# Performance work log

Hardware: AMD Instinct MI355X
Metric: run time of the kernel (lower is better)

## Reference

```python
import jax, jax.numpy as jnp
import numpy as np

D_MODEL = 1024
NUM_HEADS = 16
D_K = D_MODEL // NUM_HEADS
THETA = 10000.0


def _rope(x, pos):
    # x: [H, B, S, D_K]; pos: [S] int. Interleaved-pair rotation (matrix-form RoPE).
    d2 = D_K // 2
    inv_freq = THETA ** (-(2.0 * jnp.arange(d2, dtype=jnp.float32)) / D_K)  # [d2]
    ang = pos.astype(jnp.float32)[:, None] * inv_freq[None, :]              # [S, d2]
    sin, cos = jnp.sin(ang), jnp.cos(ang)
    xr = x.reshape(*x.shape[:-1], d2, 2)
    x0, x1 = xr[..., 0], xr[..., 1]
    out0 = cos * x0 - sin * x1
    out1 = sin * x0 + cos * x1
    return jnp.stack([out0, out1], axis=-1).reshape(x.shape)


def setup_inputs() -> dict:
    key = jax.random.key(0)
    ks = jax.random.split(key, 5)
    scale = 1.0 / np.sqrt(D_MODEL)
    return {
        "x": jax.random.normal(ks[0], (4, 2048, D_MODEL), dtype=jnp.float32),
        "token_positions": jnp.arange(2048, dtype=jnp.int32),
        "Wq": jax.random.normal(ks[1], (D_MODEL, D_MODEL), dtype=jnp.float32) * scale,
        "Wk": jax.random.normal(ks[2], (D_MODEL, D_MODEL), dtype=jnp.float32) * scale,
        "Wv": jax.random.normal(ks[3], (D_MODEL, D_MODEL), dtype=jnp.float32) * scale,
        "Wo": jax.random.normal(ks[4], (D_MODEL, D_MODEL), dtype=jnp.float32) * scale,
    }


def reference(x, token_positions, Wq, Wk, Wv, Wo):
    B, S, D = x.shape
    H, dk = NUM_HEADS, D_K
    # Projections (Linear stores weight [out,in], applies x @ W.T)
    def proj(W):
        return (x @ W.T).reshape(B, S, H, dk).transpose(2, 0, 1, 3)  # [H,B,S,dk]
    q, k, v = proj(Wq), proj(Wk), proj(Wv)
    q = _rope(q, token_positions)
    k = _rope(k, token_positions)
    scores = jnp.einsum("hbsd,hbtd->hbst", q, k) / jnp.sqrt(jnp.float32(dk))
    causal = jnp.tril(jnp.ones((S, S), dtype=bool))
    scores = jnp.where(causal, scores, jnp.float32(-1e9))
    attn = jax.nn.softmax(scores, axis=-1)
    out = jnp.einsum("hbst,hbtd->hbsd", attn, v)       # [H,B,S,dk]
    out = out.transpose(1, 2, 0, 3).reshape(B, S, D)   # [B,S,D]
    return out @ Wo.T
```

## Files before the change

### kernel.cpp

```cpp
#include <hip/hip_runtime.h>

typedef __bf16 bf16;
typedef bf16 bf16x8 __attribute__((ext_vector_type(8)));
typedef bf16 bf16x4 __attribute__((ext_vector_type(4)));
typedef float floatx4 __attribute__((ext_vector_type(4)));

#define D_MODEL 1024
#define SEQ     2048
#define NB      4
#define NH      16
#define DKH     64
#define ROPE_L2 0.4152410118609203f

__device__ __forceinline__ floatx4 mfma16(bf16x8 a, bf16x8 b, floatx4 c) {
  return __builtin_amdgcn_mfma_f32_16x16x32_bf16(a, b, c, 0, 0, 0);
}

__device__ __forceinline__ void gload_lds16(void* lds_uniform, const void* gsrc) {
  __builtin_amdgcn_global_load_lds(
      (__attribute__((address_space(1))) unsigned int*)(void*)(gsrc),
      (__attribute__((address_space(3))) unsigned int*)lds_uniform,
      16, 0, 0);
}

__global__ __launch_bounds__(256) void cvt_all(
    const float4* __restrict__ x,
    const float4* __restrict__ wq, const float4* __restrict__ wk,
    const float4* __restrict__ wv, const float4* __restrict__ wo,
    bf16x4* __restrict__ xb,
    bf16x4* __restrict__ b0, bf16x4* __restrict__ b1,
    bf16x4* __restrict__ b2, bf16x4* __restrict__ b3) {
  const int i = blockIdx.x * 256 + threadIdx.x;
  const float4* src;
  bf16x4* dst;
  int off;
  if (i < (1 << 21)) {
    src = x; dst = xb; off = i;
  } else {
    const int j = i - (1 << 21);
    const int widx = j >> 18;
    off = j & ((1 << 18) - 1);
    src = (widx == 0) ? wq : (widx == 1) ? wk : (widx == 2) ? wv : wo;
    dst = (widx == 0) ? b0 : (widx == 1) ? b1 : (widx == 2) ? b2 : b3;
  }
  const float4 v = src[off];
  bf16x4 o;
  o[0] = (bf16)v.x; o[1] = (bf16)v.y; o[2] = (bf16)v.z; o[3] = (bf16)v.w;
  dst[off] = o;
}

__global__ __launch_bounds__(256) void rope_table(const int* __restrict__ tokpos,
                                                  float2* __restrict__ tab) {
  const int i = blockIdx.x * 256 + threadIdx.x;
  const int s = i >> 5, i2 = i & 31;
  const float ang = (float)tokpos[s] * exp2f(-(float)i2 * ROPE_L2);
  float sn, cs;
  sincosf(ang, &sn, &cs);
  tab[i] = make_float2(sn, cs);
}

#define GEMM_ACC_DECL                              \
  floatx4 c00 = {}, c01 = {}, c02 = {}, c03 = {};  \
  floatx4 c10 = {}, c11 = {}, c12 = {}, c13 = {};  \
  floatx4 c20 = {}, c21 = {}, c22 = {}, c23 = {};  \
  floatx4 c30 = {}, c31 = {}, c32 = {}, c33 = {};

#define AS_BASE(buf) ((char*)LDSBUF + (buf) * 8192)
#define BS_BASE(buf) ((char*)LDSBUF + 16384 + (buf) * 8192)

#define GEMM_STAGE(buf, kk)                                                    \
  gload_lds16(AS_BASE(buf) + (w * 64) * 16, asrc0 + (kk));                     \
  gload_lds16(BS_BASE(buf) + (w * 64) * 16, bsrc0 + (kk));                     \
  gload_lds16(AS_BASE(buf) + (w * 64 + 256) * 16, asrc1 + (kk));               \
  gload_lds16(BS_BASE(buf) + (w * 64 + 256) * 16, bsrc1 + (kk));

#define GEMM_MAINLOOP(Aptr, Bptr)                                              \
  const int c_0 = w * 64 + lane;                                               \
  const int row0_ = c_0 >> 2, seg0_ = (c_0 & 3) ^ ((row0_ >> 1) & 3);          \
  const int c_1 = c_0 + 256;                                                   \
  const int row1_ = c_1 >> 2, seg1_ = (c_1 & 3) ^ ((row1_ >> 1) & 3);          \
  const bf16* asrc0 = (Aptr) + (size_t)(bm + row0_) * D_MODEL + seg0_ * 8;     \
  const bf16* asrc1 = (Aptr) + (size_t)(bm + row1_) * D_MODEL + seg1_ * 8;     \
  const bf16* bsrc0 = (Bptr) + (size_t)(bn + row0_) * D_MODEL + seg0_ * 8;     \
  const bf16* bsrc1 = (Bptr) + (size_t)(bn + row1_) * D_MODEL + seg1_ * 8;     \
  const int gsw = (g ^ ((r >> 1) & 3)) * 8;                                    \
  GEMM_STAGE(0, 0)                                                             \
  __syncthreads();                                                             \
  int cub = 0;                                                                 \
  for (int kt = 0; kt < 32; ++kt) {                                            \
    if (kt + 1 < 32) { GEMM_STAGE(cub ^ 1, (kt + 1) * 32) }                    \
    const bf16* Abase = (const bf16*)AS_BASE(cub) + (wr * 64 + r) * 32 + gsw;  \
    const bf16* Bbase = (const bf16*)BS_BASE(cub) + (wc * 64 + r) * 32 + gsw;  \
    bf16x8 a0 = *(const bf16x8*)(Abase + 0 * 512);                             \
    bf16x8 a1 = *(const bf16x8*)(Abase + 1 * 512);                             \
    bf16x8 a2 = *(const bf16x8*)(Abase + 2 * 512);                             \
    bf16x8 a3 = *(const bf16x8*)(Abase + 3 * 512);                             \
    bf16x8 b0 = *(const bf16x8*)(Bbase + 0 * 512);                             \
    bf16x8 b1 = *(const bf16x8*)(Bbase + 1 * 512);                             \
    bf16x8 b2 = *(const bf16x8*)(Bbase + 2 * 512);                             \
    bf16x8 b3 = *(const bf16x8*)(Bbase + 3 * 512);                             \
    __builtin_amdgcn_s_setprio(1);                                             \
    c00 = mfma16(a0, b0, c00); c01 = mfma16(a0, b1, c01);                      \
    c02 = mfma16(a0, b2, c02); c03 = mfma16(a0, b3, c03);                      \
    c10 = mfma16(a1, b0, c10); c11 = mfma16(a1, b1, c11);                      \
    c12 = mfma16(a1, b2, c12); c13 = mfma16(a1, b3, c13);                      \
    c20 = mfma16(a2, b0, c20); c21 = mfma16(a2, b1, c21);                      \
    c22 = mfma16(a2, b2, c22); c23 = mfma16(a2, b3, c23);                      \
    c30 = mfma16(a3, b0, c30); c31 = mfma16(a3, b1, c31);                      \
    c32 = mfma16(a3, b2, c32); c33 = mfma16(a3, b3, c33);                      \
    __builtin_amdgcn_s_setprio(0);                                             \
    __syncthreads();                                                           \
    cub ^= 1;                                                                  \
  }

#define QKV_WRITE(mm, nn, CV)                                                  \
  _Pragma("unroll")                                                            \
  for (int reg = 0; reg < 4; ++reg) {                                          \
    const int srow = mm * 16 + g * 4 + reg;                                    \
    const int c = wc * 64 + nn * 16 + r;                                       \
    const int s_ = (bm + wr * 64 + srow) & (SEQ - 1);                          \
    const int d_ = c & 63;                                                     \
    float v = CV[reg];                                                         \
    float pp = __shfl_xor(v, 1);                                               \
    const float2 sc2 = ropetab[s_ * 32 + (d_ >> 1)];                           \
    float res = ((d_ & 1) == 0) ? (sc2.y * v - sc2.x * pp)                     \
                                : (sc2.x * pp + sc2.y * v);                    \
    if (z == 0) res *= 0.125f;                                                 \
    *(bf16*)((char*)LDSBUF + srow * 272 + c * 2) = (bf16)res;                  \
  }

#define V_WRITE(mm, nn, CV)                                                    \
  _Pragma("unroll")                                                            \
  for (int reg = 0; reg < 4; ++reg) {                                          \
    const int crow = nn * 16 + r;                                              \
    const int s_l = wr * 64 + mm * 16 + g * 4 + reg;                           \
    *(bf16*)((char*)LDSBUF + crow * 272 + s_l * 2) = (bf16)CV[reg];            \
  }

__global__ __launch_bounds__(256, 3) void gemm_qkv(
    const bf16* __restrict__ A,
    const bf16* __restrict__ W0, const bf16* __restrict__ W1, const bf16* __restrict__ W2,
    bf16* __restrict__ Qd, bf16* __restrict__ Kd, bf16* __restrict__ Vd,
    const float2* __restrict__ ropetab) {
  __shared__ __align__(16) char LDSBUF[32768];
  const int orig = (int)(blockIdx.x + (blockIdx.y << 3) + (blockIdx.z << 9));
  const int l = (orig & 7) * 192 + (orig >> 3);
  const int z = l >> 9;
  const int bm = ((l >> 3) & 63) * 128, bn = (l & 7) * 128;
  const bf16* Bw = (z == 0) ? W0 : (z == 1) ? W1 : W2;
  const int tid = threadIdx.x, lane = tid & 63, w = tid >> 6;
  const int wr = w >> 1, wc = w & 1;
  const int r = lane & 15, g = lane >> 4;
  GEMM_ACC_DECL
  GEMM_MAINLOOP(A, Bw)

  const int hbase = bn >> 6;
  if (z < 2) {
    bf16* dst0 = (z == 0) ? Qd : Kd;
#pragma unroll
    for (int p = 0; p < 2; ++p) {
      if (wr == p) {
        QKV_WRITE(0, 0, c00) QKV_WRITE(0, 1, c01) QKV_WRITE(0, 2, c02) QKV_WRITE(0, 3, c03)
        QKV_WRITE(1, 0, c10) QKV_WRITE(1, 1, c11) QKV_WRITE(1, 2, c12) QKV_WRITE(1, 3, c13)
        QKV_WRITE(2, 0, c20) QKV_WRITE(2, 1, c21) QKV_WRITE(2, 2, c22) QKV_WRITE(2, 3, c23)
        QKV_WRITE(3, 0, c30) QKV_WRITE(3, 1, c31) QKV_WRITE(3, 2, c32) QKV_WRITE(3, 3, c33)
      }
      __syncthreads();
      const int s_r = tid >> 2, quad = tid & 3;
      const int grow = bm + p * 64 + s_r;
      const int b_ = grow >> 11, s_ = grow & (SEQ - 1);
      const int h_ = hbase + (quad >> 1);
      bf16* dstp = dst0 + ((size_t)(b_ * NH + h_) * SEQ + s_) * DKH + (quad & 1) * 32;
#pragma unroll
      for (int j = 0; j < 4; ++j)
        *(float4*)(dstp + j * 8) =
            *(const float4*)((char*)LDSBUF + s_r * 272 + quad * 64 + j * 16);
      __syncthreads();
    }
  } else {
    const int b_ = bm >> 11, sbase = bm & (SEQ - 1);
#pragma unroll
    for (int p = 0; p < 2; ++p) {
      if (wc == p) {
        V_WRITE(0, 0, c00) V_WRITE(0, 1, c01) V_WRITE(0, 2, c02) V_WRITE(0, 3, c03)
        V_WRITE(1, 0, c10) V_WRITE(1, 1, c11) V_WRITE(1, 2, c12) V_WRITE(1, 3, c13)
        V_WRITE(2, 0, c20) V_WRITE(2, 1, c21) V_WRITE(2, 2, c22) V_WRITE(2, 3, c23)
        V_WRITE(3, 0, c30) V_WRITE(3, 1, c31) V_WRITE(3, 2, c32) V_WRITE(3, 3, c33)
      }
      __syncthreads();
      const int c_r = tid >> 2, quad = tid & 3;
      const int c = p * 64 + c_r;
      const int h_ = hbase + (c >> 6), d_ = c & 63;
      bf16* dstp = Vd + ((size_t)(b_ * NH + h_) * DKH + d_) * SEQ + sbase + quad * 32;
#pragma unroll
      for (int j = 0; j < 4; ++j)
        *(float4*)(dstp + j * 8) =
            *(const float4*)((char*)LDSBUF + c_r * 272 + quad * 64 + j * 16);
      __syncthreads();
    }
  }
}

#define OUT_EPI(mm, nn, CV)                                                    \
  _Pragma("unroll")                                                            \
  for (int reg = 0; reg < 4; ++reg) {                                          \
    const int grow = bm + wr * 64 + mm * 16 + g * 4 + reg;                     \
    const int gcol = bn + wc * 64 + nn * 16 + r;                               \
    C[(size_t)grow * D_MODEL + gcol] = CV[reg];                                \
  }

__global__ __launch_bounds__(256, 3) void gemm_out(const bf16* __restrict__ A,
                                                   const bf16* __restrict__ Bw,
                                                   float* __restrict__ C) {
  __shared__ __align__(16) char LDSBUF[32768];
  const int orig = (int)(blockIdx.x + (blockIdx.y << 3));
  const int l = (orig & 7) * 64 + (orig >> 3);
  const int bm = (l >> 3) * 128, bn = (l & 7) * 128;
  const int tid = threadIdx.x, lane = tid & 63, w = tid >> 6;
  const int wr = w >> 1, wc = w & 1;
  const int r = lane & 15, g = lane >> 4;
  GEMM_ACC_DECL
  GEMM_MAINLOOP(A, Bw)
  OUT_EPI(0, 0, c00) OUT_EPI(0, 1, c01) OUT_EPI(0, 2, c02) OUT_EPI(0, 3, c03)
  OUT_EPI(1, 0, c10) OUT_EPI(1, 1, c11) OUT_EPI(1, 2, c12) OUT_EPI(1, 3, c13)
  OUT_EPI(2, 0, c20) OUT_EPI(2, 1, c21) OUT_EPI(2, 2, c22) OUT_EPI(2, 3, c23)
  OUT_EPI(3, 0, c30) OUT_EPI(3, 1, c31) OUT_EPI(3, 2, c32) OUT_EPI(3, 3, c33)
}

__global__ __launch_bounds__(256, 3) void attn128(const bf16* __restrict__ Q,
                                                  const bf16* __restrict__ Kk,
                                                  const bf16* __restrict__ Vt,
                                                  bf16* __restrict__ AO) {
  const int orig = (int)(blockIdx.x + (blockIdx.y << 4));
  const int i_ = orig >> 3;
  const int qt = 15 - (i_ >> 3);
  const int bh = (orig & 7) * 8 + (i_ & 7);
  const int b = bh >> 4, h = bh & 15;
  const int tid = threadIdx.x, lane = tid & 63, w = tid >> 6;
  const int r = lane & 15, g = lane >> 4;
  const int q0 = qt * 128 + w * 32;

  const bf16* Qb = Q + (size_t)bh * SEQ * DKH;
  const bf16* Kb = Kk + (size_t)bh * SEQ * DKH;
  const bf16* Vb = Vt + (size_t)bh * DKH * SEQ;

  __shared__ bf16 Ks[2][64 * 64];
  __shared__ bf16 Vs[2][64 * 64];
  __shared__ bf16 Ps[4][32 * 64];

  int ldsoff[2];
  const char* ksrc[2];
  const char* vsrc[2];
#pragma unroll
  for (int j = 0; j < 2; ++j) {
    const int L = (w * 64 + lane + 256 * j) * 16;
    const int S = L ^ (((L >> 7) & 7) << 4);
    ldsoff[j] = (w * 64 + 256 * j) * 16;
    ksrc[j] = (const char*)Kb + S;
    vsrc[j] = (const char*)Vb + (size_t)(S >> 7) * (SEQ * 2) + (S & 127);
  }

#define ATTN_STAGE(buf, tt)                                                   \
  _Pragma("unroll")                                                           \
  for (int j = 0; j < 2; ++j) {                                               \
    gload_lds16((char*)Ks[buf] + ldsoff[j], ksrc[j] + (size_t)(tt) * 8192);   \
    gload_lds16((char*)Vs[buf] + ldsoff[j], vsrc[j] + (size_t)(tt) * 128);    \
  }

#define SM_TILE(MASKED)                                                        \
  _Pragma("unroll")                                                            \
  for (int m = 0; m < 2; ++m) {                                                \
    const int qq_ = q0 + m * 16 + r;                                           \
    const int wl_ = m * 16 + r;                                                \
    _Pragma("unroll")                                                          \
    for (int nf = 0; nf < 4; ++nf) {                                           \
      floatx4 p;                                                               \
      _Pragma("unroll")                                                        \
      for (int reg = 0; reg < 4; ++reg) {                                      \
        float pe = exp2f(fmaf(sc[m][nf][reg], 1.442695041f, -17.31234049f));   \
        if (MASKED && (t0 + nf * 16 + g * 4 + reg > qq_)) pe = 0.f;            \
        p[reg] = pe;                                                           \
      }                                                                        \
      l2[m] += p;                                                              \
      unsigned u0, u1;                                                         \
      asm("v_cvt_pk_bf16_f32 %0, %1, %2" : "=v"(u0) : "v"(p[0]), "v"(p[1]));   \
      asm("v_cvt_pk_bf16_f32 %0, %1, %2" : "=v"(u1) : "v"(p[2]), "v"(p[3]));   \
      const int pb = (wl_ * 128 + nf * 32 + g * 8) ^ ((wl_ & 7) << 4);         \
      *(uint2*)((char*)Ps[w] + pb) = make_uint2(u0, u1);                       \
    }                                                                          \
  }

  bf16x8 qf[2][2];
#pragma unroll
  for (int m = 0; m < 2; ++m)
#pragma unroll
    for (int ks = 0; ks < 2; ++ks)
      qf[m][ks] = *(const bf16x8*)(Qb + (size_t)(q0 + m * 16 + r) * DKH + ks * 32 + g * 8);

  floatx4 o[2][4] = {};
  floatx4 l2[2] = {};

  const int nt = 2 * qt + 2;
  ATTN_STAGE(0, 0)
  __syncthreads();
  int cu = 0;
  for (int t = 0; t < nt; ++t) {
    if (t + 1 < nt) ATTN_STAGE(cu ^ 1, t + 1)
    const int t0 = t * 64;

    floatx4 sc[2][4];
    __builtin_amdgcn_s_setprio(1);
#pragma unroll
    for (int nf = 0; nf < 4; ++nf) {
      const int row = nf * 16 + r;
      const int off0 = (row * 128 + g * 16) ^ ((row & 7) << 4);
      bf16x8 kf0 = *(const bf16x8*)((const char*)Ks[cu] + off0);
      bf16x8 kf1 = *(const bf16x8*)((const char*)Ks[cu] + (off0 ^ 64));
      sc[0][nf] = mfma16(kf1, qf[0][1], mfma16(kf0, qf[0][0], floatx4{0.f, 0.f, 0.f, 0.f}));
      sc[1][nf] = mfma16(kf1, qf[1][1], mfma16(kf0, qf[1][0], floatx4{0.f, 0.f, 0.f, 0.f}));
    }
    __builtin_amdgcn_s_setprio(0);

    const bool edge = (t0 + 63 > q0);
    if (edge) {
      SM_TILE(1)
    } else {
      SM_TILE(0)
    }
    asm volatile("s_waitcnt lgkmcnt(0)" ::: "memory");

    bf16x8 pf[2][2];
#pragma unroll
    for (int m = 0; m < 2; ++m)
#pragma unroll
      for (int ks = 0; ks < 2; ++ks) {
        const int prow = m * 16 + r;
        const int ab = (prow * 128 + ks * 64 + g * 16) ^ ((prow & 7) << 4);
        pf[m][ks] = *(const bf16x8*)((const char*)Ps[w] + ab);
      }
    __builtin_amdgcn_s_setprio(1);
#pragma unroll
    for (int nf = 0; nf < 4; ++nf) {
      const int vrow = nf * 16 + r;
      const int vb0 = (vrow * 128 + g * 16) ^ ((vrow & 7) << 4);
      bf16x8 vf0 = *(const bf16x8*)((const char*)Vs[cu] + vb0);
      bf16x8 vf1 = *(const bf16x8*)((const char*)Vs[cu] + (vb0 ^ 64));
#pragma unroll
      for (int m = 0; m < 2; ++m)
        o[m][nf] = mfma16(pf[m][1], vf1, mfma16(pf[m][0], vf0, o[m][nf]));
    }
    __builtin_amdgcn_s_setprio(0);
    __syncthreads();
    cu ^= 1;
  }

  float lsm[2];
#pragma unroll
  for (int m = 0; m < 2; ++m) {
    float ls = l2[m][0] + l2[m][1] + l2[m][2] + l2[m][3];
    ls += __shfl_xor(ls, 16);
    ls += __shfl_xor(ls, 32);
    lsm[m] = ls;
  }
  float linv[2][4];
#pragma unroll
  for (int m = 0; m < 2; ++m)
#pragma unroll
    for (int reg = 0; reg < 4; ++reg)
      linv[m][reg] = 1.f / __shfl(lsm[m], g * 4 + reg);

#pragma unroll
  for (int m = 0; m < 2; ++m)
#pragma unroll
    for (int nf = 0; nf < 4; ++nf)
#pragma unroll
      for (int reg = 0; reg < 4; ++reg) {
        const int s = q0 + m * 16 + g * 4 + reg;
        const int d = nf * 16 + r;
        const float val = o[m][nf][reg] * linv[m][reg];
        AO[((size_t)(b * SEQ + s)) * D_MODEL + h * DKH + d] = (bf16)val;
      }
}

extern "C" void kernel_launch(void* const* d_in, const int* in_sizes, int n_in,
                              void* d_out, int out_size, void* d_ws, size_t ws_size,
                              hipStream_t stream) {
  const float* x = (const float*)d_in[0];
  const int* tokpos = (const int*)d_in[1];
  const float* Wq = (const float*)d_in[2];
  const float* Wk = (const float*)d_in[3];
  const float* Wv = (const float*)d_in[4];
  const float* Wo = (const float*)d_in[5];
  float* out = (float*)d_out;

  char* ws = (char*)d_ws;
  if (ws_size < (72ull << 20)) return;

  bf16* xb  = (bf16*)(ws);
  bf16* wb0 = (bf16*)(ws + (16ull << 20));
  bf16* wb1 = (bf16*)(ws + (18ull << 20));
  bf16* wb2 = (bf16*)(ws + (20ull << 20));
  bf16* wb3 = (bf16*)(ws + (22ull << 20));
  bf16* Qb  = (bf16*)(ws + (24ull << 20));
  bf16* Kb  = (bf16*)(ws + (40ull << 20));
  bf16* Vt  = (bf16*)(ws + (56ull << 20));
  bf16* AO  = (bf16*)(ws);
  float2* ropetab = (float2*)d_out;

  rope_table<<<256, 256, 0, stream>>>(tokpos, ropetab);
  cvt_all<<<12288, 256, 0, stream>>>((const float4*)x, (const float4*)Wq,
                                     (const float4*)Wk, (const float4*)Wv,
                                     (const float4*)Wo, (bf16x4*)xb,
                                     (bf16x4*)wb0, (bf16x4*)wb1,
                                     (bf16x4*)wb2, (bf16x4*)wb3);

  gemm_qkv<<<dim3(8, 64, 3), 256, 0, stream>>>(xb, wb0, wb1, wb2, Qb, Kb, Vt, ropetab);
  attn128<<<dim3(16, 64), 256, 0, stream>>>(Qb, Kb, Vt, AO);
  gemm_out<<<dim3(8, 64), 256, 0, stream>>>(AO, wb3, out);
}
```

Measured before the change: 178.8 us.

## Split QKV GEMM into fused Q+K kernel sharing A tiles and separate V kernel

Replaces the single QKV GEMM launch with a Q+K kernel in which each block loads one A tile and computes both the Q and K outputs, and a separate V GEMM kernel. The aim is to halve A-operand loads for Q and K and to raise MFMA work per LDS A read. In exchange the Q+K kernel uses twice the accumulators and 48KB of LDS, dropping occupancy to 2 blocks per CU, and it adds one more kernel launch.

Result: no change. 178.6 us (-0.1%).

```diff
diff --git a/kernel.cpp b/kernel.cpp
--- a/kernel.cpp
+++ b/kernel.cpp
@@ -57,6 +57,145 @@
   float sn, cs;
   sincosf(ang, &sn, &cs);
   tab[i] = make_float2(sn, cs);
+}
+
+#define QK_SRC_DECL(Aptr, Bq, Bk)                                              \
+  const int c_0 = w * 64 + lane;                                               \
+  const int row0_ = c_0 >> 2, seg0_ = (c_0 & 3) ^ ((row0_ >> 1) & 3);          \
+  const int c_1 = c_0 + 256;                                                   \
+  const int row1_ = c_1 >> 2, seg1_ = (c_1 & 3) ^ ((row1_ >> 1) & 3);          \
+  const bf16* asrc0 = (Aptr) + (size_t)(bm + row0_) * D_MODEL + seg0_ * 8;     \
+  const bf16* asrc1 = (Aptr) + (size_t)(bm + row1_) * D_MODEL + seg1_ * 8;     \
+  const bf16* bqsrc0 = (Bq) + (size_t)(bn + row0_) * D_MODEL + seg0_ * 8;      \
+  const bf16* bqsrc1 = (Bq) + (size_t)(bn + row1_) * D_MODEL + seg1_ * 8;      \
+  const bf16* bksrc0 = (Bk) + (size_t)(bn + row0_) * D_MODEL + seg0_ * 8;      \
+  const bf16* bksrc1 = (Bk) + (size_t)(bn + row1_) * D_MODEL + seg1_ * 8;     \
+  const int gsw = (g ^ ((r >> 1) & 3)) * 8;
+
+#define QKA(buf) ((char*)LDSBUF + (buf) * 8192)
+#define QKQ(buf) ((char*)LDSBUF + 16384 + (buf) * 8192)
+#define QKK(buf) ((char*)LDSBUF + 32768 + (buf) * 8192)
+
+#define QK_STAGE(buf, kk)                                                      \
+  gload_lds16(QKA(buf) + (w * 64) * 16, asrc0 + (kk));                         \
+  gload_lds16(QKQ(buf) + (w * 64) * 16, bqsrc0 + (kk));                        \
+  gload_lds16(QKK(buf) + (w * 64) * 16, bksrc0 + (kk));                        \
+  gload_lds16(QKA(buf) + (w * 64 + 256) * 16, asrc1 + (kk));                   \
+  gload_lds16(QKQ(buf) + (w * 64 + 256) * 16, bqsrc1 + (kk));                  \
+  gload_lds16(QKK(buf) + (w * 64 + 256) * 16, bksrc1 + (kk));
+
+#define ROPEW(mm, nn, CV, SC)                                                  \
+  _Pragma("unroll")                                                            \
+  for (int reg = 0; reg < 4; ++reg) {                                          \
+    const int srow = mm * 16 + g * 4 + reg;                                    \
+    const int c = wc * 64 + nn * 16 + r;                                       \
+    const int s_ = (bm + wr * 64 + srow) & (SEQ - 1);                          \
+    const int d_ = c & 63;                                                     \
+    float v = CV[reg];                                                         \
+    float pp = __shfl_xor(v, 1);                                               \
+    const float2 sc2 = ropetab[s_ * 32 + (d_ >> 1)];                           \
+    float res = ((d_ & 1) == 0) ? (sc2.y * v - sc2.x * pp)                     \
+                                : (sc2.x * pp + sc2.y * v);                    \
+    res *= SC;                                                                 \
+    *(bf16*)((char*)LDSBUF + srow * 272 + c * 2) = (bf16)res;                  \
+  }
+
+#define QK_EPI(A00,A01,A02,A03,A10,A11,A12,A13,A20,A21,A22,A23,A30,A31,A32,A33,\
+               dst0, SC)                                                       \
+  _Pragma("unroll")                                                            \
+  for (int p = 0; p < 2; ++p) {                                                \
+    if (wr == p) {                                                             \
+      ROPEW(0, 0, A00, SC) ROPEW(0, 1, A01, SC) ROPEW(0, 2, A02, SC)           \
+      ROPEW(0, 3, A03, SC) ROPEW(1, 0, A10, SC) ROPEW(1, 1, A11, SC)           \
+      ROPEW(1, 2, A12, SC) ROPEW(1, 3, A13, SC) ROPEW(2, 0, A20, SC)           \
+      ROPEW(2, 1, A21, SC) ROPEW(2, 2, A22, SC) ROPEW(2, 3, A23, SC)           \
+      ROPEW(3, 0, A30, SC) ROPEW(3, 1, A31, SC) ROPEW(3, 2, A32, SC)           \
+      ROPEW(3, 3, A33, SC)                                                     \
+    }                                                                          \
+    __syncthreads();                                                           \
+    const int s_r = tid >> 2, quad = tid & 3;                                  \
+    const int grow = bm + p * 64 + s_r;                                        \
+    const int b_ = grow >> 11, s_ = grow & (SEQ - 1);                          \
+    const int h_ = hbase + (quad >> 1);                                        \
+    bf16* dstp = (dst0) + ((size_t)(b_ * NH + h_) * SEQ + s_) * DKH +          \
+                 (quad & 1) * 32;                                              \
+    _Pragma("unroll")                                                          \
+    for (int j = 0; j < 4; ++j)                                                \
+      *(float4*)(dstp + j * 8) =                                               \
+          *(const float4*)((char*)LDSBUF + s_r * 272 + quad * 64 + j * 16);    \
+    __syncthreads();                                                           \
+  }
+
+__global__ __launch_bounds__(256, 2) void gemm_qk(
+    const bf16* __restrict__ A,
+    const bf16* __restrict__ Wq, const bf16* __restrict__ Wk,
+    bf16* __restrict__ Qd, bf16* __restrict__ Kd,
+    const float2* __restrict__ ropetab) {
+  __shared__ __align__(16) char LDSBUF[49152];
+  const int orig = (int)(blockIdx.x + (blockIdx.y << 3));
+  const int l = (orig & 7) * 64 + (orig >> 3);
+  const int bm = (l >> 3) * 128, bn = (l & 7) * 128;
+  const int tid = threadIdx.x, lane = tid & 63, w = tid >> 6;
+  const int wr = w >> 1, wc = w & 1;
+  const int r = lane & 15, g = lane >> 4;
+
+  floatx4 q00 = {}, q01 = {}, q02 = {}, q03 = {};
+  floatx4 q10 = {}, q11 = {}, q12 = {}, q13 = {};
+  floatx4 q20 = {}, q21 = {}, q22 = {}, q23 = {};
+  floatx4 q30 = {}, q31 = {}, q32 = {}, q33 = {};
+  floatx4 k00 = {}, k01 = {}, k02 = {}, k03 = {};
+  floatx4 k10 = {}, k11 = {}, k12 = {}, k13 = {};
+  floatx4 k20 = {}, k21 = {}, k22 = {}, k23 = {};
+  floatx4 k30 = {}, k31 = {}, k32 = {}, k33 = {};
+
+  QK_SRC_DECL(A, Wq, Wk)
+  QK_STAGE(0, 0)
+  __syncthreads();
+  int cub = 0;
+  for (int kt = 0; kt < 32; ++kt) {
+    if (kt + 1 < 32) { QK_STAGE(cub ^ 1, (kt + 1) * 32) }
+    const bf16* Abase = (const bf16*)QKA(cub) + (wr * 64 + r) * 32 + gsw;
+    const bf16* Qbase = (const bf16*)QKQ(cub) + (wc * 64 + r) * 32 + gsw;
+    const bf16* Kbase = (const bf16*)QKK(cub) + (wc * 64 + r) * 32 + gsw;
+    bf16x8 a0 = *(const bf16x8*)(Abase + 0 * 512);
+    bf16x8 a1 = *(const bf16x8*)(Abase + 1 * 512);
+    bf16x8 a2 = *(const bf16x8*)(Abase + 2 * 512);
+    bf16x8 a3 = *(const bf16x8*)(Abase + 3 * 512);
+    bf16x8 bq0 = *(const bf16x8*)(Qbase + 0 * 512);
+    bf16x8 bq1 = *(const bf16x8*)(Qbase + 1 * 512);
+    bf16x8 bq2 = *(const bf16x8*)(Qbase + 2 * 512);
+    bf16x8 bq3 = *(const bf16x8*)(Qbase + 3 * 512);
+    bf16x8 bk0 = *(const bf16x8*)(Kbase + 0 * 512);
+    bf16x8 bk1 = *(const bf16x8*)(Kbase + 1 * 512);
+    bf16x8 bk2 = *(const bf16x8*)(Kbase + 2 * 512);
+    bf16x8 bk3 = *(const bf16x8*)(Kbase + 3 * 512);
+    __builtin_amdgcn_s_setprio(1);
+    q00 = mfma16(a0, bq0, q00); q01 = mfma16(a0, bq1, q01);
+    q02 = mfma16(a0, bq2, q02); q03 = mfma16(a0, bq3, q03);
+    k00 = mfma16(a0, bk0, k00); k01 = mfma16(a0, bk1, k01);
+    k02 = mfma16(a0, bk2, k02); k03 = mfma16(a0, bk3, k03);
+    q10 = mfma16(a1, bq0, q10); q11 = mfma16(a1, bq1, q11);
+    q12 = mfma16(a1, bq2, q12); q13 = mfma16(a1, bq3, q13);
+    k10 = mfma16(a1, bk0, k10); k11 = mfma16(a1, bk1, k11);
+    k12 = mfma16(a1, bk2, k12); k13 = mfma16(a1, bk3, k13);
+    q20 = mfma16(a2, bq0, q20); q21 = mfma16(a2, bq1, q21);
+    q22 = mfma16(a2, bq2, q22); q23 = mfma16(a2, bq3, q23);
+    k20 = mfma16(a2, bk0, k20); k21 = mfma16(a2, bk1, k21);
+    k22 = mfma16(a2, bk2, k22); k23 = mfma16(a2, bk3, k23);
+    q30 = mfma16(a3, bq0, q30); q31 = mfma16(a3, bq1, q31);
+    q32 = mfma16(a3, bq2, q32); q33 = mfma16(a3, bq3, q33);
+    k30 = mfma16(a3, bk0, k30); k31 = mfma16(a3, bk1, k31);
+    k32 = mfma16(a3, bk2, k32); k33 = mfma16(a3, bk3, k33);
+    __builtin_amdgcn_s_setprio(0);
+    __syncthreads();
+    cub ^= 1;
+  }
+
+  const int hbase = bn >> 6;
+  QK_EPI(q00,q01,q02,q03,q10,q11,q12,q13,q20,q21,q22,q23,q30,q31,q32,q33,
+         Qd, 0.125f)
+  QK_EPI(k00,k01,k02,k03,k10,k11,k12,k13,k20,k21,k22,k23,k30,k31,k32,k33,
+         Kd, 1.0f)
 }
 
 #define GEMM_ACC_DECL                              \
@@ -113,22 +252,6 @@
     cub ^= 1;                                                                  \
   }
 
-#define QKV_WRITE(mm, nn, CV)                                                  \
-  _Pragma("unroll")                                                            \
-  for (int reg = 0; reg < 4; ++reg) {                                          \
-    const int srow = mm * 16 + g * 4 + reg;                                    \
-    const int c = wc * 64 + nn * 16 + r;                                       \
-    const int s_ = (bm + wr * 64 + srow) & (SEQ - 1);                          \
-    const int d_ = c & 63;                                                     \
-    float v = CV[reg];                                                         \
-    float pp = __shfl_xor(v, 1);                                               \
-    const float2 sc2 = ropetab[s_ * 32 + (d_ >> 1)];                           \
-    float res = ((d_ & 1) == 0) ? (sc2.y * v - sc2.x * pp)                     \
-                                : (sc2.x * pp + sc2.y * v);                    \
-    if (z == 0) res *= 0.125f;                                                 \
-    *(bf16*)((char*)LDSBUF + srow * 272 + c * 2) = (bf16)res;                  \
-  }
-
 #define V_WRITE(mm, nn, CV)                                                    \
   _Pragma("unroll")                                                            \
   for (int reg = 0; reg < 4; ++reg) {                                          \
@@ -137,67 +260,39 @@
     *(bf16*)((char*)LDSBUF + crow * 272 + s_l * 2) = (bf16)CV[reg];            \
   }
 
-__global__ __launch_bounds__(256, 3) void gemm_qkv(
-    const bf16* __restrict__ A,
-    const bf16* __restrict__ W0, const bf16* __restrict__ W1, const bf16* __restrict__ W2,
-    bf16* __restrict__ Qd, bf16* __restrict__ Kd, bf16* __restrict__ Vd,
-    const float2* __restrict__ ropetab) {
+__global__ __launch_bounds__(256, 3) void gemm_v(const bf16* __restrict__ A,
+                                                 const bf16* __restrict__ Wv,
+                                                 bf16* __restrict__ Vd) {
   __shared__ __align__(16) char LDSBUF[32768];
-  const int orig = (int)(blockIdx.x + (blockIdx.y << 3) + (blockIdx.z << 9));
-  const int l = (orig & 7) * 192 + (orig >> 3);
-  const int z = l >> 9;
-  const int bm = ((l >> 3) & 63) * 128, bn = (l & 7) * 128;
-  const bf16* Bw = (z == 0) ? W0 : (z == 1) ? W1 : W2;
+  const int orig = (int)(blockIdx.x + (blockIdx.y << 3));
+  const int l = (orig & 7) * 64 + (orig >> 3);
+  const int bm = (l >> 3) * 128, bn = (l & 7) * 128;
   const int tid = threadIdx.x, lane = tid & 63, w = tid >> 6;
   const int wr = w >> 1, wc = w & 1;
   const int r = lane & 15, g = lane >> 4;
   GEMM_ACC_DECL
-  GEMM_MAINLOOP(A, Bw)
+  GEMM_MAINLOOP(A, Wv)
 
   const int hbase = bn >> 6;
-  if (z < 2) {
-    bf16* dst0 = (z == 0) ? Qd : Kd;
-#pragma unroll
-    for (int p = 0; p < 2; ++p) {
-      if (wr == p) {
-        QKV_WRITE(0, 0, c00) QKV_WRITE(0, 1, c01) QKV_WRITE(0, 2, c02) QKV_WRITE(0, 3, c03)
-        QKV_WRITE(1, 0, c10) QKV_WRITE(1, 1, c11) QKV_WRITE(1, 2, c12) QKV_WRITE(1, 3, c13)
-        QKV_WRITE(2, 0, c20) QKV_WRITE(2, 1, c21) QKV_WRITE(2, 2, c22) QKV_WRITE(2, 3, c23)
-        QKV_WRITE(3, 0, c30) QKV_WRITE(3, 1, c31) QKV_WRITE(3, 2, c32) QKV_WRITE(3, 3, c33)
-      }
-      __syncthreads();
-      const int s_r = tid >> 2, quad = tid & 3;
-      const int grow = bm + p * 64 + s_r;
-      const int b_ = grow >> 11, s_ = grow & (SEQ - 1);
-      const int h_ = hbase + (quad >> 1);
-      bf16* dstp = dst0 + ((size_t)(b_ * NH + h_) * SEQ + s_) * DKH + (quad & 1) * 32;
-#pragma unroll
-      for (int j = 0; j < 4; ++j)
-        *(float4*)(dstp + j * 8) =
-            *(const float4*)((char*)LDSBUF + s_r * 272 + quad * 64 + j * 16);
-      __syncthreads();
+  const int b_ = bm >> 11, sbase = bm & (SEQ - 1);
+#pragma unroll
+  for (int p = 0; p < 2; ++p) {
+    if (wc == p) {
+      V_WRITE(0, 0, c00) V_WRITE(0, 1, c01) V_WRITE(0, 2, c02) V_WRITE(0, 3, c03)
+      V_WRITE(1, 0, c10) V_WRITE(1, 1, c11) V_WRITE(1, 2, c12) V_WRITE(1, 3, c13)
+      V_WRITE(2, 0, c20) V_WRITE(2, 1, c21) V_WRITE(2, 2, c22) V_WRITE(2, 3, c23)
+      V_WRITE(3, 0, c30) V_WRITE(3, 1, c31) V_WRITE(3, 2, c32) V_WRITE(3, 3, c33)
     }
-  } else {
-    const int b_ = bm >> 11, sbase = bm & (SEQ - 1);
-#pragma unroll
-    for (int p = 0; p < 2; ++p) {
-      if (wc == p) {
-        V_WRITE(0, 0, c00) V_WRITE(0, 1, c01) V_WRITE(0, 2, c02) V_WRITE(0, 3, c03)
-        V_WRITE(1, 0, c10) V_WRITE(1, 1, c11) V_WRITE(1, 2, c12) V_WRITE(1, 3, c13)
-        V_WRITE(2, 0, c20) V_WRITE(2, 1, c21) V_WRITE(2, 2, c22) V_WRITE(2, 3, c23)
-        V_WRITE(3, 0, c30) V_WRITE(3, 1, c31) V_WRITE(3, 2, c32) V_WRITE(3, 3, c33)
-      }
-      __syncthreads();
-      const int c_r = tid >> 2, quad = tid & 3;
-      const int c = p * 64 + c_r;
-      const int h_ = hbase + (c >> 6), d_ = c & 63;
-      bf16* dstp = Vd + ((size_t)(b_ * NH + h_) * DKH + d_) * SEQ + sbase + quad * 32;
-#pragma unroll
-      for (int j = 0; j < 4; ++j)
-        *(float4*)(dstp + j * 8) =
-            *(const float4*)((char*)LDSBUF + c_r * 272 + quad * 64 + j * 16);
-      __syncthreads();
-    }
+    __syncthreads();
+    const int c_r = tid >> 2, quad = tid & 3;
+    const int c = p * 64 + c_r;
+    const int h_ = hbase + (c >> 6), d_ = c & 63;
+    bf16* dstp = Vd + ((size_t)(b_ * NH + h_) * DKH + d_) * SEQ + sbase + quad * 32;
+#pragma unroll
+    for (int j = 0; j < 4; ++j)
+      *(float4*)(dstp + j * 8) =
+          *(const float4*)((char*)LDSBUF + c_r * 272 + quad * 64 + j * 16);
+    __syncthreads();
   }
 }
 
@@ -414,7 +509,8 @@
                                      (bf16x4*)wb0, (bf16x4*)wb1,
                                      (bf16x4*)wb2, (bf16x4*)wb3);
 
-  gemm_qkv<<<dim3(8, 64, 3), 256, 0, stream>>>(xb, wb0, wb1, wb2, Qb, Kb, Vt, ropetab);
+  gemm_qk<<<dim3(8, 64), 256, 0, stream>>>(xb, wb0, wb1, Qb, Kb, ropetab);
+  gemm_v<<<dim3(8, 64), 256, 0, stream>>>(xb, wb2, Vt);
   attn128<<<dim3(16, 64), 256, 0, stream>>>(Qb, Kb, Vt, AO);
   gemm_out<<<dim3(8, 64), 256, 0, stream>>>(AO, wb3, out);
 }
```
